# Kernel optimization log

Hardware: AMD Instinct MI355X
Metric: run time of the kernel (lower is better)

The kernel has to match this reference:

```python
import jax, jax.numpy as jnp
import numpy as np

TEMPERATURE = 0.1
EPS = 1e-12  # F.normalize default eps


def _l2norm(x):
    n = jnp.sqrt(jnp.sum(x * x, axis=-1, keepdims=True))
    return x / jnp.maximum(n, EPS)


def setup_inputs() -> dict:
    key = jax.random.key(0)
    k1, k2, k3 = jax.random.split(key, 3)
    G, NA, NO, D = 256, 256, 512, 128
    student_nodes = jax.random.normal(k1, (G * NA, D), dtype=jnp.float32)
    teacher_nodes = jax.random.normal(k2, (G * NO, D), dtype=jnp.float32)
    # local indices into each original graph's node block (as in t_nodes_all[kept_indices])
    kept_node_indices = jax.random.randint(k3, (G * NA,), 0, NO, dtype=jnp.int64)
    return {
        "student_nodes": student_nodes,
        "teacher_nodes": teacher_nodes,
        "kept_node_indices": kept_node_indices,
        "num_graphs": G,
        "n_aug": NA,
        "n_orig": NO,
    }


def reference(student_nodes, teacher_nodes, kept_node_indices, num_graphs, n_aug, n_orig):
    D = student_nodes.shape[-1]
    # ragged batch regularized: ptr boundaries -> fixed-size reshape
    s = _l2norm(student_nodes.reshape(num_graphs, n_aug, D))      # [G, Na, D]
    t = _l2norm(teacher_nodes.reshape(num_graphs, n_orig, D))     # [G, No, D]
    kept = kept_node_indices.reshape(num_graphs, n_aug)           # [G, Na]
    t_aligned = jnp.take_along_axis(t, kept[:, :, None], axis=1)  # [G, Na, D]
    scores = jnp.einsum("gid,gjd->gij", s, t_aligned) / TEMPERATURE  # [G, Na, Na]
    logp = jax.nn.log_softmax(scores, axis=-1)
    idx = jnp.arange(n_aug)
    # CE with labels = arange: -logp[g, i, i], mean over i per graph, then mean over graphs
    per_graph_ce = -jnp.mean(logp[:, idx, idx], axis=-1)          # [G]
    return jnp.mean(per_graph_ce)
```

## Files before the change

kernel.cpp:

```cpp
#include <hip/hip_runtime.h>
#include <hip/hip_bf16.h>

using f32x4  = __attribute__((ext_vector_type(4))) float;
using bf16x8 = __attribute__((ext_vector_type(8))) short;

constexpr int   G_NUM = 256;
constexpr int   NAUG  = 256;
constexpr int   NORIG = 512;
constexpr int   DIM   = 128;
constexpr float INV_T = 10.0f;
constexpr int   NBLK  = 256;

constexpr int PAIR_PITCH = 1040;
constexpr int STAGE_BYTES = 64 * PAIR_PITCH;

__device__ __forceinline__ short f32_to_bf16_bits(float x) {
    unsigned u = __float_as_uint(x);
    u += 0x7fffu + ((u >> 16) & 1u);
    return (short)(u >> 16);
}

__global__ __launch_bounds__(512, 2) void nlcl_main(
    const float* __restrict__ student,
    const float* __restrict__ teacher,
    const int*   __restrict__ kept,
    float*       __restrict__ block_sums)
{
    __shared__ __align__(16) char  stage[STAGE_BYTES];
    __shared__ __align__(16) short tile[NAUG * DIM];
    __shared__ float red[8];

    const int g    = blockIdx.x;
    const int tid  = threadIdx.x;
    const int lane = tid & 63;
    const int wave = tid >> 6;

    const float* s_base = student + (size_t)g * NAUG * DIM;
    const float* t_base = teacher + (size_t)g * NORIG * DIM;
    const int*   k_base = kept + g * NAUG;

    const int ccol  = lane & 15;
    const int cquad = lane >> 4;

    int srcv[16];
    #pragma unroll
    for (int t = 0; t < 16; ++t) {
        const int pair = (t >> 3) * 64 + wave * 8 + (t & 7);
        srcv[t] = k_base[pair * 2 + (lane >> 5)];
    }

    float4 sv[16];
    #pragma unroll
    for (int rt = 0; rt < 2; ++rt) {
        const float* rp = s_base + (wave * 32 + rt * 16 + ccol) * DIM;
        #pragma unroll
        for (int kc = 0; kc < 4; ++kc) {
            sv[rt * 8 + kc * 2]     = *reinterpret_cast<const float4*>(rp + kc * 32 + cquad * 8);
            sv[rt * 8 + kc * 2 + 1] = *reinterpret_cast<const float4*>(rp + kc * 32 + cquad * 8 + 4);
        }
    }

    #pragma unroll
    for (int i = 0; i < 8; ++i) {
        const float* src = t_base + (size_t)srcv[i] * DIM + (lane & 31) * 4;
        char* dst = stage + (wave * 8 + i) * PAIR_PITCH;
        __builtin_amdgcn_global_load_lds(
            (const __attribute__((address_space(1))) void*)src,
            (__attribute__((address_space(3))) void*)dst, 16, 0, 0);
    }

    bf16x8 afrag[2][4];
    #pragma unroll
    for (int rt = 0; rt < 2; ++rt) {
        float ss = 0.f;
        #pragma unroll
        for (int q = 0; q < 8; ++q) {
            const float4 v = sv[rt * 8 + q];
            ss += v.x * v.x + v.y * v.y + v.z * v.z + v.w * v.w;
        }
        ss += __shfl_xor(ss, 16);
        ss += __shfl_xor(ss, 32);
        const float scale = rsqrtf(fmaxf(ss, 1e-24f));
        #pragma unroll
        for (int kc = 0; kc < 4; ++kc) {
            const float4 a = sv[rt * 8 + kc * 2], b = sv[rt * 8 + kc * 2 + 1];
            afrag[rt][kc][0] = f32_to_bf16_bits(a.x * scale);
            afrag[rt][kc][1] = f32_to_bf16_bits(a.y * scale);
            afrag[rt][kc][2] = f32_to_bf16_bits(a.z * scale);
            afrag[rt][kc][3] = f32_to_bf16_bits(a.w * scale);
            afrag[rt][kc][4] = f32_to_bf16_bits(b.x * scale);
            afrag[rt][kc][5] = f32_to_bf16_bits(b.y * scale);
            afrag[rt][kc][6] = f32_to_bf16_bits(b.z * scale);
            afrag[rt][kc][7] = f32_to_bf16_bits(b.w * scale);
        }
    }

    __syncthreads();

    char* tb = reinterpret_cast<char*>(tile);
    {
        const int row_l = tid >> 2;
        const int sub   = tid & 3;
        const int j     = row_l;
        const char* sp = stage + (row_l >> 1) * PAIR_PITCH + (row_l & 1) * 512 + sub * 128;
        float vals[32]; float ss = 0.f;
        #pragma unroll
        for (int it = 0; it < 8; ++it) {
            const float4 v = *reinterpret_cast<const float4*>(sp + it * 16);
            vals[it * 4] = v.x; vals[it * 4 + 1] = v.y;
            vals[it * 4 + 2] = v.z; vals[it * 4 + 3] = v.w;
            ss += v.x * v.x + v.y * v.y + v.z * v.z + v.w * v.w;
        }
        ss += __shfl_xor(ss, 1);
        ss += __shfl_xor(ss, 2);
        const float scale = rsqrtf(fmaxf(ss, 1e-24f));
        #pragma unroll
        for (int p = 0; p < 4; ++p) {
            bf16x8 o;
            #pragma unroll
            for (int e = 0; e < 8; ++e) o[e] = f32_to_bf16_bits(vals[p * 8 + e] * scale);
            const int byte = j * 256 + ((sub * 64 + p * 16) ^ ((j & 7) << 4));
            *reinterpret_cast<bf16x8*>(tb + byte) = o;
        }
    }
    __syncthreads();

    #pragma unroll
    for (int i = 0; i < 8; ++i) {
        const float* src = t_base + (size_t)srcv[8 + i] * DIM + (lane & 31) * 4;
        char* dst = stage + (wave * 8 + i) * PAIR_PITCH;
        __builtin_amdgcn_global_load_lds(
            (const __attribute__((address_space(1))) void*)src,
            (__attribute__((address_space(3))) void*)dst, 16, 0, 0);
    }

    float sumexp[2][4] = {{0.f,0.f,0.f,0.f},{0.f,0.f,0.f,0.f}};
    float diagsum = 0.f;
    const char* tlc = reinterpret_cast<const char*>(tile);

    #pragma unroll 2
    for (int ct = 0; ct < 8; ++ct) {
        f32x4 acc0 = {0.f,0.f,0.f,0.f};
        f32x4 acc1 = {0.f,0.f,0.f,0.f};
        const int j = ct * 16 + ccol;
        #pragma unroll
        for (int kc = 0; kc < 4; ++kc) {
            const int byte = j * 256 + (((kc * 64) + (cquad * 16)) ^ ((j & 7) << 4));
            const bf16x8 b = *reinterpret_cast<const bf16x8*>(tlc + byte);
            acc0 = __builtin_amdgcn_mfma_f32_16x16x32_bf16(afrag[0][kc], b, acc0, 0, 0, 0);
            acc1 = __builtin_amdgcn_mfma_f32_16x16x32_bf16(afrag[1][kc], b, acc1, 0, 0, 0);
        }
        #pragma unroll
        for (int reg = 0; reg < 4; ++reg) {
            const int row0 = wave * 32 + cquad * 4 + reg;
            const int row1 = row0 + 16;
            const float l0 = acc0[reg] * INV_T;
            const float l1 = acc1[reg] * INV_T;
            sumexp[0][reg] += __expf(l0);
            sumexp[1][reg] += __expf(l1);
            if (j == row0) diagsum += l0;
            if (j == row1) diagsum += l1;
        }
    }
    __syncthreads();

    {
        const int row_l = tid >> 2;
        const int sub   = tid & 3;
        const int j     = 128 + row_l;
        const char* sp = stage + (row_l >> 1) * PAIR_PITCH + (row_l & 1) * 512 + sub * 128;
        float vals[32]; float ss = 0.f;
        #pragma unroll
        for (int it = 0; it < 8; ++it) {
            const float4 v = *reinterpret_cast<const float4*>(sp + it * 16);
            vals[it * 4] = v.x; vals[it * 4 + 1] = v.y;
            vals[it * 4 + 2] = v.z; vals[it * 4 + 3] = v.w;
            ss += v.x * v.x + v.y * v.y + v.z * v.z + v.w * v.w;
        }
        ss += __shfl_xor(ss, 1);
        ss += __shfl_xor(ss, 2);
        const float scale = rsqrtf(fmaxf(ss, 1e-24f));
        #pragma unroll
        for (int p = 0; p < 4; ++p) {
            bf16x8 o;
            #pragma unroll
            for (int e = 0; e < 8; ++e) o[e] = f32_to_bf16_bits(vals[p * 8 + e] * scale);
            const int byte = j * 256 + ((sub * 64 + p * 16) ^ ((j & 7) << 4));
            *reinterpret_cast<bf16x8*>(tb + byte) = o;
        }
    }
    __syncthreads();

    #pragma unroll 2
    for (int ct = 8; ct < 16; ++ct) {
        f32x4 acc0 = {0.f,0.f,0.f,0.f};
        f32x4 acc1 = {0.f,0.f,0.f,0.f};
        const int j = ct * 16 + ccol;
        #pragma unroll
        for (int kc = 0; kc < 4; ++kc) {
            const int byte = j * 256 + (((kc * 64) + (cquad * 16)) ^ ((j & 7) << 4));
            const bf16x8 b = *reinterpret_cast<const bf16x8*>(tlc + byte);
            acc0 = __builtin_amdgcn_mfma_f32_16x16x32_bf16(afrag[0][kc], b, acc0, 0, 0, 0);
            acc1 = __builtin_amdgcn_mfma_f32_16x16x32_bf16(afrag[1][kc], b, acc1, 0, 0, 0);
        }
        #pragma unroll
        for (int reg = 0; reg < 4; ++reg) {
            const int row0 = wave * 32 + cquad * 4 + reg;
            const int row1 = row0 + 16;
            const float l0 = acc0[reg] * INV_T;
            const float l1 = acc1[reg] * INV_T;
            sumexp[0][reg] += __expf(l0);
            sumexp[1][reg] += __expf(l1);
            if (j == row0) diagsum += l0;
            if (j == row1) diagsum += l1;
        }
    }

    float ce = 0.f;
    #pragma unroll
    for (int rt = 0; rt < 2; ++rt) {
        #pragma unroll
        for (int reg = 0; reg < 4; ++reg) {
            float s = sumexp[rt][reg];
            s += __shfl_xor(s, 1);
            s += __shfl_xor(s, 2);
            s += __shfl_xor(s, 4);
            s += __shfl_xor(s, 8);
            if (ccol == 0) ce += __logf(s);
        }
    }
    ce -= diagsum;
    ce += __shfl_xor(ce, 1);
    ce += __shfl_xor(ce, 2);
    ce += __shfl_xor(ce, 4);
    ce += __shfl_xor(ce, 8);
    ce += __shfl_xor(ce, 16);
    ce += __shfl_xor(ce, 32);

    if (lane == 0) red[wave] = ce;
    __syncthreads();
    if (tid == 0) {
        float t = 0.f;
        #pragma unroll
        for (int w = 0; w < 8; ++w) t += red[w];
        block_sums[g] = t;
    }
}

__global__ void nlcl_reduce(const float* __restrict__ block_sums,
                            float* __restrict__ out)
{
    __shared__ float r[4];
    const int tid = threadIdx.x;
    float v = block_sums[tid];
    v += __shfl_xor(v, 1);
    v += __shfl_xor(v, 2);
    v += __shfl_xor(v, 4);
    v += __shfl_xor(v, 8);
    v += __shfl_xor(v, 16);
    v += __shfl_xor(v, 32);
    if ((tid & 63) == 0) r[tid >> 6] = v;
    __syncthreads();
    if (tid == 0)
        out[0] = (r[0] + r[1] + r[2] + r[3]) * (1.0f / ((float)G_NUM * (float)NAUG));
}

extern "C" void kernel_launch(void* const* d_in, const int* in_sizes, int n_in,
                              void* d_out, int out_size, void* d_ws, size_t ws_size,
                              hipStream_t stream) {
    (void)in_sizes; (void)n_in; (void)out_size; (void)ws_size;
    const float* student = (const float*)d_in[0];
    const float* teacher = (const float*)d_in[1];
    const int*   kept    = (const int*)d_in[2];
    float* bs  = (float*)d_ws;
    float* out = (float*)d_out;

    nlcl_main<<<NBLK, 512, 0, stream>>>(student, teacher, kept, bs);
    nlcl_reduce<<<1, 256, 0, stream>>>(bs, out);
}
```

Before: 23.16 us.

## Pipeline teacher gather in four quarters with double-buffered LDS staging

```diff
diff --git a/kernel.cpp b/kernel.cpp
--- a/kernel.cpp
+++ b/kernel.cpp
@@ -12,7 +12,8 @@
 constexpr int   NBLK  = 256;
 
 constexpr int PAIR_PITCH = 1040;
-constexpr int STAGE_BYTES = 64 * PAIR_PITCH;
+constexpr int SLOT_BYTES = 32 * PAIR_PITCH;
+constexpr int STAGE_BYTES = 2 * SLOT_BYTES;
 
 __device__ __forceinline__ short f32_to_bf16_bits(float x) {
     unsigned u = __float_as_uint(x);
@@ -45,7 +46,7 @@
     int srcv[16];
     #pragma unroll
     for (int t = 0; t < 16; ++t) {
-        const int pair = (t >> 3) * 64 + wave * 8 + (t & 7);
+        const int pair = (t >> 2) * 32 + wave * 4 + (t & 3);
         srcv[t] = k_base[pair * 2 + (lane >> 5)];
     }
 
@@ -60,14 +61,48 @@
         }
     }
 
-    #pragma unroll
-    for (int i = 0; i < 8; ++i) {
-        const float* src = t_base + (size_t)srcv[i] * DIM + (lane & 31) * 4;
-        char* dst = stage + (wave * 8 + i) * PAIR_PITCH;
-        __builtin_amdgcn_global_load_lds(
-            (const __attribute__((address_space(1))) void*)src,
-            (__attribute__((address_space(3))) void*)dst, 16, 0, 0);
-    }
+    auto dma_quarter = [&](int k) {
+        #pragma unroll
+        for (int i = 0; i < 4; ++i) {
+            const float* src = t_base + (size_t)srcv[k * 4 + i] * DIM + (lane & 31) * 4;
+            char* dst = stage + (k & 1) * SLOT_BYTES + (wave * 4 + i) * PAIR_PITCH;
+            __builtin_amdgcn_global_load_lds(
+                (const __attribute__((address_space(1))) void*)src,
+                (__attribute__((address_space(3))) void*)dst, 16, 0, 0);
+        }
+    };
+
+    auto convert_quarter = [&](int k) {
+        const int row_l = tid >> 3;
+        const int sub   = tid & 7;
+        const int j     = k * 64 + row_l;
+        const char* sp = stage + (k & 1) * SLOT_BYTES
+                       + (row_l >> 1) * PAIR_PITCH + (row_l & 1) * 512 + sub * 64;
+        float vals[16]; float ss = 0.f;
+        #pragma unroll
+        for (int it = 0; it < 4; ++it) {
+            const float4 v = *reinterpret_cast<const float4*>(sp + it * 16);
+            vals[it * 4] = v.x; vals[it * 4 + 1] = v.y;
+            vals[it * 4 + 2] = v.z; vals[it * 4 + 3] = v.w;
+            ss += v.x * v.x + v.y * v.y + v.z * v.z + v.w * v.w;
+        }
+        ss += __shfl_xor(ss, 1);
+        ss += __shfl_xor(ss, 2);
+        ss += __shfl_xor(ss, 4);
+        const float scale = rsqrtf(fmaxf(ss, 1e-24f));
+        char* tb = reinterpret_cast<char*>(tile);
+        #pragma unroll
+        for (int p = 0; p < 2; ++p) {
+            bf16x8 o;
+            #pragma unroll
+            for (int e = 0; e < 8; ++e) o[e] = f32_to_bf16_bits(vals[p * 8 + e] * scale);
+            const int byte = j * 256 + ((sub * 32 + p * 16) ^ ((j & 7) << 4));
+            *reinterpret_cast<bf16x8*>(tb + byte) = o;
+        }
+    };
+
+    dma_quarter(0);
+    dma_quarter(1);
 
     bf16x8 afrag[2][4];
     #pragma unroll
@@ -95,126 +130,66 @@
         }
     }
 
-    __syncthreads();
-
-    char* tb = reinterpret_cast<char*>(tile);
-    {
-        const int row_l = tid >> 2;
-        const int sub   = tid & 3;
-        const int j     = row_l;
-        const char* sp = stage + (row_l >> 1) * PAIR_PITCH + (row_l & 1) * 512 + sub * 128;
-        float vals[32]; float ss = 0.f;
-        #pragma unroll
-        for (int it = 0; it < 8; ++it) {
-            const float4 v = *reinterpret_cast<const float4*>(sp + it * 16);
-            vals[it * 4] = v.x; vals[it * 4 + 1] = v.y;
-            vals[it * 4 + 2] = v.z; vals[it * 4 + 3] = v.w;
-            ss += v.x * v.x + v.y * v.y + v.z * v.z + v.w * v.w;
-        }
-        ss += __shfl_xor(ss, 1);
-        ss += __shfl_xor(ss, 2);
-        const float scale = rsqrtf(fmaxf(ss, 1e-24f));
-        #pragma unroll
-        for (int p = 0; p < 4; ++p) {
-            bf16x8 o;
-            #pragma unroll
-            for (int e = 0; e < 8; ++e) o[e] = f32_to_bf16_bits(vals[p * 8 + e] * scale);
-            const int byte = j * 256 + ((sub * 64 + p * 16) ^ ((j & 7) << 4));
-            *reinterpret_cast<bf16x8*>(tb + byte) = o;
-        }
-    }
-    __syncthreads();
-
-    #pragma unroll
-    for (int i = 0; i < 8; ++i) {
-        const float* src = t_base + (size_t)srcv[8 + i] * DIM + (lane & 31) * 4;
-        char* dst = stage + (wave * 8 + i) * PAIR_PITCH;
-        __builtin_amdgcn_global_load_lds(
-            (const __attribute__((address_space(1))) void*)src,
-            (__attribute__((address_space(3))) void*)dst, 16, 0, 0);
-    }
-
     float sumexp[2][4] = {{0.f,0.f,0.f,0.f},{0.f,0.f,0.f,0.f}};
     float diagsum = 0.f;
     const char* tlc = reinterpret_cast<const char*>(tile);
 
-    #pragma unroll 2
-    for (int ct = 0; ct < 8; ++ct) {
-        f32x4 acc0 = {0.f,0.f,0.f,0.f};
-        f32x4 acc1 = {0.f,0.f,0.f,0.f};
-        const int j = ct * 16 + ccol;
-        #pragma unroll
-        for (int kc = 0; kc < 4; ++kc) {
-            const int byte = j * 256 + (((kc * 64) + (cquad * 16)) ^ ((j & 7) << 4));
-            const bf16x8 b = *reinterpret_cast<const bf16x8*>(tlc + byte);
-            acc0 = __builtin_amdgcn_mfma_f32_16x16x32_bf16(afrag[0][kc], b, acc0, 0, 0, 0);
-            acc1 = __builtin_amdgcn_mfma_f32_16x16x32_bf16(afrag[1][kc], b, acc1, 0, 0, 0);
-        }
-        #pragma unroll
-        for (int reg = 0; reg < 4; ++reg) {
-            const int row0 = wave * 32 + cquad * 4 + reg;
-            const int row1 = row0 + 16;
-            const float l0 = acc0[reg] * INV_T;
-            const float l1 = acc1[reg] * INV_T;
-            sumexp[0][reg] += __expf(l0);
-            sumexp[1][reg] += __expf(l1);
-            if (j == row0) diagsum += l0;
-            if (j == row1) diagsum += l1;
-        }
-    }
-    __syncthreads();
-
-    {
-        const int row_l = tid >> 2;
-        const int sub   = tid & 3;
-        const int j     = 128 + row_l;
-        const char* sp = stage + (row_l >> 1) * PAIR_PITCH + (row_l & 1) * 512 + sub * 128;
-        float vals[32]; float ss = 0.f;
-        #pragma unroll
-        for (int it = 0; it < 8; ++it) {
-            const float4 v = *reinterpret_cast<const float4*>(sp + it * 16);
-            vals[it * 4] = v.x; vals[it * 4 + 1] = v.y;
-            vals[it * 4 + 2] = v.z; vals[it * 4 + 3] = v.w;
-            ss += v.x * v.x + v.y * v.y + v.z * v.z + v.w * v.w;
-        }
-        ss += __shfl_xor(ss, 1);
-        ss += __shfl_xor(ss, 2);
-        const float scale = rsqrtf(fmaxf(ss, 1e-24f));
-        #pragma unroll
-        for (int p = 0; p < 4; ++p) {
-            bf16x8 o;
+    auto mfma_quarter = [&](int k) {
+        #pragma unroll
+        for (int ct = 4 * k; ct < 4 * k + 4; ++ct) {
+            f32x4 acc0 = {0.f,0.f,0.f,0.f};
+            f32x4 acc1 = {0.f,0.f,0.f,0.f};
+            const int j = ct * 16 + ccol;
             #pragma unroll
-            for (int e = 0; e < 8; ++e) o[e] = f32_to_bf16_bits(vals[p * 8 + e] * scale);
-            const int byte = j * 256 + ((sub * 64 + p * 16) ^ ((j & 7) << 4));
-            *reinterpret_cast<bf16x8*>(tb + byte) = o;
-        }
-    }
-    __syncthreads();
-
-    #pragma unroll 2
-    for (int ct = 8; ct < 16; ++ct) {
-        f32x4 acc0 = {0.f,0.f,0.f,0.f};
-        f32x4 acc1 = {0.f,0.f,0.f,0.f};
-        const int j = ct * 16 + ccol;
-        #pragma unroll
-        for (int kc = 0; kc < 4; ++kc) {
-            const int byte = j * 256 + (((kc * 64) + (cquad * 16)) ^ ((j & 7) << 4));
-            const bf16x8 b = *reinterpret_cast<const bf16x8*>(tlc + byte);
-            acc0 = __builtin_amdgcn_mfma_f32_16x16x32_bf16(afrag[0][kc], b, acc0, 0, 0, 0);
-            acc1 = __builtin_amdgcn_mfma_f32_16x16x32_bf16(afrag[1][kc], b, acc1, 0, 0, 0);
-        }
-        #pragma unroll
-        for (int reg = 0; reg < 4; ++reg) {
-            const int row0 = wave * 32 + cquad * 4 + reg;
-            const int row1 = row0 + 16;
-            const float l0 = acc0[reg] * INV_T;
-            const float l1 = acc1[reg] * INV_T;
-            sumexp[0][reg] += __expf(l0);
-            sumexp[1][reg] += __expf(l1);
-            if (j == row0) diagsum += l0;
-            if (j == row1) diagsum += l1;
-        }
-    }
+            for (int kc = 0; kc < 4; ++kc) {
+                const int byte = j * 256 + (((kc * 64) + (cquad * 16)) ^ ((j & 7) << 4));
+                const bf16x8 b = *reinterpret_cast<const bf16x8*>(tlc + byte);
+                acc0 = __builtin_amdgcn_mfma_f32_16x16x32_bf16(afrag[0][kc], b, acc0, 0, 0, 0);
+                acc1 = __builtin_amdgcn_mfma_f32_16x16x32_bf16(afrag[1][kc], b, acc1, 0, 0, 0);
+            }
+            #pragma unroll
+            for (int reg = 0; reg < 4; ++reg) {
+                const int row0 = wave * 32 + cquad * 4 + reg;
+                const int row1 = row0 + 16;
+                const float l0 = acc0[reg] * INV_T;
+                const float l1 = acc1[reg] * INV_T;
+                sumexp[0][reg] += __expf(l0);
+                sumexp[1][reg] += __expf(l1);
+                if (j == row0) diagsum += l0;
+                if (j == row1) diagsum += l1;
+            }
+        }
+    };
+
+    asm volatile("s_waitcnt vmcnt(4)" ::: "memory");
+    __builtin_amdgcn_s_barrier();
+    convert_quarter(0);
+    asm volatile("s_waitcnt lgkmcnt(0)" ::: "memory");
+    __builtin_amdgcn_s_barrier();
+    dma_quarter(2);
+    mfma_quarter(0);
+
+    asm volatile("s_waitcnt vmcnt(4)" ::: "memory");
+    __builtin_amdgcn_s_barrier();
+    convert_quarter(1);
+    asm volatile("s_waitcnt lgkmcnt(0)" ::: "memory");
+    __builtin_amdgcn_s_barrier();
+    dma_quarter(3);
+    mfma_quarter(1);
+
+    asm volatile("s_waitcnt vmcnt(4)" ::: "memory");
+    __builtin_amdgcn_s_barrier();
+    convert_quarter(2);
+    asm volatile("s_waitcnt lgkmcnt(0)" ::: "memory");
+    __builtin_amdgcn_s_barrier();
+    mfma_quarter(2);
+
+    asm volatile("s_waitcnt vmcnt(0)" ::: "memory");
+    __builtin_amdgcn_s_barrier();
+    convert_quarter(3);
+    asm volatile("s_waitcnt lgkmcnt(0)" ::: "memory");
+    __builtin_amdgcn_s_barrier();
+    mfma_quarter(3);
 
     float ce = 0.f;
     #pragma unroll
```

After: 22.97 us (median of 2 runs). Within noise of the previous version (-0.8%).
